# Performance work log

Hardware: AMD Instinct MI355X
Metric: run time of the kernel (lower is better)

## Reference

```python
import jax, jax.numpy as jnp
import numpy as np

B, T_CACHE, N_STATE, N_HEAD = 128, 448, 1280, 20
HEAD_DIM = N_STATE // N_HEAD


def setup_inputs() -> dict:
    key = jax.random.key(0)
    ks = jax.random.split(key, 10)
    s = 1.0 / np.sqrt(N_STATE)
    return {
        "x": jax.random.normal(ks[0], (B, 1, N_STATE), jnp.float32),
        "k_cache": jax.random.normal(ks[1], (B, T_CACHE, N_STATE), jnp.float32),
        "v_cache": jax.random.normal(ks[2], (B, T_CACHE, N_STATE), jnp.float32),
        "mask": jnp.zeros((1, T_CACHE), jnp.float32),
        "Wq": jax.random.normal(ks[3], (N_STATE, N_STATE), jnp.float32) * s,
        "bq": jax.random.normal(ks[4], (N_STATE,), jnp.float32) * s,
        "Wk": jax.random.normal(ks[5], (N_STATE, N_STATE), jnp.float32) * s,
        "Wv": jax.random.normal(ks[6], (N_STATE, N_STATE), jnp.float32) * s,
        "bv": jax.random.normal(ks[7], (N_STATE,), jnp.float32) * s,
        "Wo": jax.random.normal(ks[8], (N_STATE, N_STATE), jnp.float32) * s,
        "bo": jax.random.normal(ks[9], (N_STATE,), jnp.float32) * s,
    }


def reference(x, k_cache, v_cache, mask, Wq, bq, Wk, Wv, bv, Wo, bo):
    b, q_len, n_state = x.shape  # q_len == 1 in loop (streaming) mode
    h, d = N_HEAD, n_state // N_HEAD

    # Q/K/V projections (Whisper: key has no bias)
    q = x @ Wq + bq                         # [B, 1, n_state]
    k = x @ Wk                              # [B, 1, n_state]
    v = x @ Wv + bv                         # [B, 1, n_state]

    # streaming KV-cache shift-and-append
    k_cache = jnp.concatenate([k_cache[:, 1:, :], k], axis=1)  # [B, T, n_state]
    v_cache = jnp.concatenate([v_cache[:, 1:, :], v], axis=1)

    t = k_cache.shape[1]
    scale = d ** (-0.25)
    qh = q.reshape(b, q_len, h, d).transpose(0, 2, 1, 3) * scale   # [B, H, q, d]
    kh = k_cache.reshape(b, t, h, d).transpose(0, 2, 3, 1) * scale  # [B, H, d, T]
    vh = v_cache.reshape(b, t, h, d).transpose(0, 2, 1, 3)          # [B, H, T, d]

    qk = jnp.matmul(qh, kh) + mask          # [B, H, q, T]
    qk = qk.astype(jnp.float32)
    w = jax.nn.softmax(qk, axis=-1).astype(qh.dtype)
    wv = jnp.matmul(w, vh)                  # [B, H, q, d]
    wv = wv.transpose(0, 2, 1, 3).reshape(b, q_len, n_state)

    out = wv @ Wo + bo                      # [B, q, n_state]
    return out, k_cache, v_cache
```

## Files before the change

kernel.cpp:

```cpp
#include <hip/hip_runtime.h>
#include <cstddef>

#define NSTATE 1280
#define TCACHE 448
#define NBATCH 128
#define NHEAD  20
#define HDIM   64
#define NT     8
#define RPC    (TCACHE / NT)

typedef float f4 __attribute__((ext_vector_type(4)));

__device__ __forceinline__ void gemm_body(const float* __restrict__ A,
                                          const float* __restrict__ B,
                                          const float* __restrict__ bias,
                                          float* __restrict__ C, size_t ldc,
                                          int kb, int ke, float scale)
{
    __shared__ float As[32][64];
    __shared__ float Bs[32][32];
    const int tid = threadIdx.x;
    const int m0 = blockIdx.y * 64;
    const int n0 = blockIdx.x * 32;
    const int tr = tid >> 4;
    const int tc = tid & 15;
    float acc[4][2] = {{0.f,0.f},{0.f,0.f},{0.f,0.f},{0.f,0.f}};

    for (int k0 = kb; k0 < ke; k0 += 32) {
        #pragma unroll
        for (int j = 0; j < 2; ++j) {
            int chunk = tid * 2 + j;
            int row   = chunk >> 3;
            int kc    = (chunk & 7) << 2;
            float4 a = *(const float4*)(A + (size_t)(m0 + row) * NSTATE + k0 + kc);
            As[kc+0][row] = a.x; As[kc+1][row] = a.y;
            As[kc+2][row] = a.z; As[kc+3][row] = a.w;
        }
        {
            int row = tid >> 3;
            int nc  = (tid & 7) << 2;
            float4 b4 = *(const float4*)(B + (size_t)(k0 + row) * NSTATE + n0 + nc);
            *(float4*)&Bs[row][nc] = b4;
        }
        __syncthreads();
        #pragma unroll
        for (int kk = 0; kk < 32; ++kk) {
            float4 a = *(const float4*)&As[kk][tr << 2];
            float2 b = *(const float2*)&Bs[kk][tc << 1];
            acc[0][0] = fmaf(a.x, b.x, acc[0][0]); acc[0][1] = fmaf(a.x, b.y, acc[0][1]);
            acc[1][0] = fmaf(a.y, b.x, acc[1][0]); acc[1][1] = fmaf(a.y, b.y, acc[1][1]);
            acc[2][0] = fmaf(a.z, b.x, acc[2][0]); acc[2][1] = fmaf(a.z, b.y, acc[2][1]);
            acc[3][0] = fmaf(a.w, b.x, acc[3][0]); acc[3][1] = fmaf(a.w, b.y, acc[3][1]);
        }
        __syncthreads();
    }
    const int n = n0 + (tc << 1);
    const float b0 = bias ? bias[n]   : 0.f;
    const float b1 = bias ? bias[n+1] : 0.f;
    #pragma unroll
    for (int i = 0; i < 4; ++i) {
        size_t m = (size_t)(m0 + (tr << 2) + i);
        C[m * ldc + n]     = (acc[i][0] + b0) * scale;
        C[m * ldc + n + 1] = (acc[i][1] + b1) * scale;
    }
}

__global__ void __launch_bounds__(256) proj_qkv_kernel(
    const float* __restrict__ x,
    const float* __restrict__ Wq, const float* __restrict__ bq,
    const float* __restrict__ Wk,
    const float* __restrict__ Wv, const float* __restrict__ bv,
    float* __restrict__ q_ws, float* __restrict__ kout, float* __restrict__ vout)
{
    const int z = blockIdx.z;
    if (z == 0) {
        gemm_body(x, Wq, bq, q_ws, NSTATE, 0, NSTATE, 0.125f);
    } else if (z == 1) {
        gemm_body(x, Wk, nullptr, kout + (size_t)(TCACHE-1) * NSTATE,
                  (size_t)TCACHE * NSTATE, 0, NSTATE, 1.0f);
    } else {
        gemm_body(x, Wv, bv, vout + (size_t)(TCACHE-1) * NSTATE,
                  (size_t)TCACHE * NSTATE, 0, NSTATE, 1.0f);
    }
}

__global__ void __launch_bounds__(320) fused_stream_kernel(
    const float* __restrict__ kin, const float* __restrict__ vin,
    const float* __restrict__ q_ws, const float* __restrict__ mask,
    float* __restrict__ kout, float* __restrict__ vout,
    float* __restrict__ pvp, float* __restrict__ m_ws, float* __restrict__ s_ws)
{
    const int tc = blockIdx.x, b = blockIdx.y;
    const int tid = threadIdx.x;
    const int h = tid >> 4, l = tid & 15;
    const int col = tid << 2;
    const size_t base = (size_t)b * TCACHE * NSTATE;
    const int t0 = tc * RPC;
    const int nrows = (tc == NT - 1) ? RPC - 1 : RPC;

    __shared__ float sc[NHEAD][RPC];

    const float4 q4 = *(const float4*)(q_ws + (size_t)b * NSTATE + col);

    {
        const float* src0 = kin + base + (size_t)(t0 + 1) * NSTATE + col;
        float* dst0 = kout + base + (size_t)t0 * NSTATE + col;
        #pragma unroll 4
        for (int r = 0; r < nrows; ++r) {
            f4 kv = __builtin_nontemporal_load((const f4*)(src0 + (size_t)r * NSTATE));
            __builtin_nontemporal_store(kv, (f4*)(dst0 + (size_t)r * NSTATE));
            float p = kv[0]*q4.x + kv[1]*q4.y + kv[2]*q4.z + kv[3]*q4.w;
            p += __shfl_xor(p, 1); p += __shfl_xor(p, 2);
            p += __shfl_xor(p, 4); p += __shfl_xor(p, 8);
            if (l == 0) sc[h][r] = p + mask[t0 + r];
        }
        if (tc == NT - 1) {
            const f4 kv = *(const f4*)(kout + base + (size_t)(TCACHE-1) * NSTATE + col);
            float p = kv[0]*q4.x + kv[1]*q4.y + kv[2]*q4.z + kv[3]*q4.w;
            p += __shfl_xor(p, 1); p += __shfl_xor(p, 2);
            p += __shfl_xor(p, 4); p += __shfl_xor(p, 8);
            if (l == 0) sc[h][RPC - 1] = p + mask[TCACHE - 1];
        }
    }
    __syncthreads();

    {
        float v[4];
        float m = -1e30f;
        #pragma unroll
        for (int j = 0; j < 4; ++j) {
            int r = l + 16 * j;
            v[j] = (r < RPC) ? sc[h][r] : -1e30f;
            m = fmaxf(m, v[j]);
        }
        #pragma unroll
        for (int d = 1; d <= 8; d <<= 1) m = fmaxf(m, __shfl_xor(m, d));
        float s = 0.f;
        #pragma unroll
        for (int j = 0; j < 4; ++j) {
            v[j] = __expf(v[j] - m);
            s += v[j];
        }
        #pragma unroll
        for (int d = 1; d <= 8; d <<= 1) s += __shfl_xor(s, d);
        __syncthreads();
        #pragma unroll
        for (int j = 0; j < 4; ++j) {
            int r = l + 16 * j;
            if (r < RPC) sc[h][r] = v[j];
        }
        if (l == 0) {
            m_ws[((size_t)b * NT + tc) * NHEAD + h] = m;
            s_ws[((size_t)b * NT + tc) * NHEAD + h] = s;
        }
    }
    __syncthreads();

    float ax = 0.f, ay = 0.f, az = 0.f, aw = 0.f;
    {
        const float* src0 = vin + base + (size_t)(t0 + 1) * NSTATE + col;
        float* dst0 = vout + base + (size_t)t0 * NSTATE + col;
        #pragma unroll 4
        for (int r = 0; r < nrows; ++r) {
            f4 vv = __builtin_nontemporal_load((const f4*)(src0 + (size_t)r * NSTATE));
            __builtin_nontemporal_store(vv, (f4*)(dst0 + (size_t)r * NSTATE));
            const float w = sc[h][r];
            ax = fmaf(w, vv[0], ax); ay = fmaf(w, vv[1], ay);
            az = fmaf(w, vv[2], az); aw = fmaf(w, vv[3], aw);
        }
        if (tc == NT - 1) {
            const f4 vv = *(const f4*)(vout + base + (size_t)(TCACHE-1) * NSTATE + col);
            const float w = sc[h][RPC - 1];
            ax = fmaf(w, vv[0], ax); ay = fmaf(w, vv[1], ay);
            az = fmaf(w, vv[2], az); aw = fmaf(w, vv[3], aw);
        }
    }
    *(float4*)(pvp + ((size_t)b * NT + tc) * NSTATE + col) =
        make_float4(ax, ay, az, aw);
}

__global__ void __launch_bounds__(256) combine_kernel(
    const float* __restrict__ pvp, const float* __restrict__ m_ws,
    const float* __restrict__ s_ws, float* __restrict__ wv_ws)
{
    const size_t idx = ((size_t)blockIdx.x * 256 + threadIdx.x) * 4;
    const int b = (int)(idx / NSTATE), col = (int)(idx % NSTATE);
    const int h = col >> 6;

    float m[NT], s[NT];
    float M = -1e30f;
    #pragma unroll
    for (int c = 0; c < NT; ++c) {
        m[c] = m_ws[((size_t)b * NT + c) * NHEAD + h];
        s[c] = s_ws[((size_t)b * NT + c) * NHEAD + h];
        M = fmaxf(M, m[c]);
    }
    float S = 0.f;
    float f[NT];
    #pragma unroll
    for (int c = 0; c < NT; ++c) { f[c] = __expf(m[c] - M); S += s[c] * f[c]; }
    const float inv = 1.0f / S;

    float4 acc = make_float4(0.f, 0.f, 0.f, 0.f);
    #pragma unroll
    for (int c = 0; c < NT; ++c) {
        const float w = f[c] * inv;
        float4 a = *(const float4*)(pvp + ((size_t)b * NT + c) * NSTATE + col);
        acc.x = fmaf(w, a.x, acc.x); acc.y = fmaf(w, a.y, acc.y);
        acc.z = fmaf(w, a.z, acc.z); acc.w = fmaf(w, a.w, acc.w);
    }
    *(float4*)(wv_ws + idx) = acc;
}

__global__ void __launch_bounds__(256) outproj_kernel(
    const float* __restrict__ wv, const float* __restrict__ Wo,
    float* __restrict__ po)
{
    const int sp = blockIdx.z;
    gemm_body(wv, Wo, nullptr, po + (size_t)sp * NBATCH * NSTATE,
              NSTATE, sp * 320, sp * 320 + 320, 1.0f);
}

__global__ void __launch_bounds__(256) out_reduce_kernel(
    const float* __restrict__ po, const float* __restrict__ bo,
    float* __restrict__ out)
{
    const size_t idx = ((size_t)blockIdx.x * 256 + threadIdx.x) * 4;
    const int col = (int)(idx % NSTATE);
    float4 s = *(const float4*)(bo + col);
    #pragma unroll
    for (int c = 0; c < 4; ++c) {
        float4 a = *(const float4*)(po + (size_t)c * NBATCH * NSTATE + idx);
        s.x += a.x; s.y += a.y; s.z += a.z; s.w += a.w;
    }
    *(float4*)(out + idx) = s;
}

extern "C" void kernel_launch(void* const* d_in, const int* in_sizes, int n_in,
                              void* d_out, int out_size, void* d_ws, size_t ws_size,
                              hipStream_t stream)
{
    const float* x       = (const float*)d_in[0];
    const float* k_cache = (const float*)d_in[1];
    const float* v_cache = (const float*)d_in[2];
    const float* mask    = (const float*)d_in[3];
    const float* Wq      = (const float*)d_in[4];
    const float* bq      = (const float*)d_in[5];
    const float* Wk      = (const float*)d_in[6];
    const float* Wv      = (const float*)d_in[7];
    const float* bv      = (const float*)d_in[8];
    const float* Wo      = (const float*)d_in[9];
    const float* bo      = (const float*)d_in[10];

    float* out  = (float*)d_out;
    float* kout = out + (size_t)NBATCH * NSTATE;
    float* vout = kout + (size_t)NBATCH * TCACHE * NSTATE;

    float* ws     = (float*)d_ws;
    float* q_ws   = ws;
    float* pvp_ws = q_ws  + (size_t)NBATCH * NSTATE;
    float* m_ws   = pvp_ws + (size_t)NBATCH * NT * NSTATE;
    float* s_ws   = m_ws  + (size_t)NBATCH * NT * NHEAD;
    float* wv_ws  = s_ws  + (size_t)NBATCH * NT * NHEAD;
    float* po_ws  = wv_ws + (size_t)NBATCH * NSTATE;

    proj_qkv_kernel<<<dim3(40, 2, 3), 256, 0, stream>>>(x, Wq, bq, Wk, Wv, bv,
                                                        q_ws, kout, vout);
    fused_stream_kernel<<<dim3(NT, NBATCH), 320, 0, stream>>>(
        k_cache, v_cache, q_ws, mask, kout, vout, pvp_ws, m_ws, s_ws);
    combine_kernel<<<dim3(160), 256, 0, stream>>>(pvp_ws, m_ws, s_ws, wv_ws);
    outproj_kernel<<<dim3(40, 2, 4), 256, 0, stream>>>(wv_ws, Wo, po_ws);
    out_reduce_kernel<<<dim3(160), 256, 0, stream>>>(po_ws, bo, out);
}
```

Measured before the change: 308.4 us.

## Use bf16 MFMA for QKV and output projections, drop split-K reduction

Replaces the fp32 LDS-tiled GEMMs for the Q/K/V and output projections with bf16 MFMA 16x16x32 kernels that convert operands on load. The combine kernel now writes the attention output directly as bf16. The out-projection no longer uses split-K, so the separate reduce kernel and its partial-sum buffer are gone and one launch is saved. The cost is bf16 rounding of weights and activations, which may hurt accuracy. Another risk is that weights are loaded with strided scalar reads and there are few blocks (60 and 20), so occupancy is low. A redundant extra load was also added in combine.

```diff
diff --git a/kernel.cpp b/kernel.cpp
--- a/kernel.cpp
+++ b/kernel.cpp
@@ -10,78 +10,103 @@
 #define RPC    (TCACHE / NT)
 
 typedef float f4 __attribute__((ext_vector_type(4)));
-
-__device__ __forceinline__ void gemm_body(const float* __restrict__ A,
-                                          const float* __restrict__ B,
-                                          const float* __restrict__ bias,
-                                          float* __restrict__ C, size_t ldc,
-                                          int kb, int ke, float scale)
-{
-    __shared__ float As[32][64];
-    __shared__ float Bs[32][32];
-    const int tid = threadIdx.x;
-    const int m0 = blockIdx.y * 64;
-    const int n0 = blockIdx.x * 32;
-    const int tr = tid >> 4;
-    const int tc = tid & 15;
-    float acc[4][2] = {{0.f,0.f},{0.f,0.f},{0.f,0.f},{0.f,0.f}};
-
-    for (int k0 = kb; k0 < ke; k0 += 32) {
-        #pragma unroll
-        for (int j = 0; j < 2; ++j) {
-            int chunk = tid * 2 + j;
-            int row   = chunk >> 3;
-            int kc    = (chunk & 7) << 2;
-            float4 a = *(const float4*)(A + (size_t)(m0 + row) * NSTATE + k0 + kc);
-            As[kc+0][row] = a.x; As[kc+1][row] = a.y;
-            As[kc+2][row] = a.z; As[kc+3][row] = a.w;
-        }
-        {
-            int row = tid >> 3;
-            int nc  = (tid & 7) << 2;
-            float4 b4 = *(const float4*)(B + (size_t)(k0 + row) * NSTATE + n0 + nc);
-            *(float4*)&Bs[row][nc] = b4;
-        }
-        __syncthreads();
-        #pragma unroll
-        for (int kk = 0; kk < 32; ++kk) {
-            float4 a = *(const float4*)&As[kk][tr << 2];
-            float2 b = *(const float2*)&Bs[kk][tc << 1];
-            acc[0][0] = fmaf(a.x, b.x, acc[0][0]); acc[0][1] = fmaf(a.x, b.y, acc[0][1]);
-            acc[1][0] = fmaf(a.y, b.x, acc[1][0]); acc[1][1] = fmaf(a.y, b.y, acc[1][1]);
-            acc[2][0] = fmaf(a.z, b.x, acc[2][0]); acc[2][1] = fmaf(a.z, b.y, acc[2][1]);
-            acc[3][0] = fmaf(a.w, b.x, acc[3][0]); acc[3][1] = fmaf(a.w, b.y, acc[3][1]);
-        }
-        __syncthreads();
-    }
-    const int n = n0 + (tc << 1);
-    const float b0 = bias ? bias[n]   : 0.f;
-    const float b1 = bias ? bias[n+1] : 0.f;
-    #pragma unroll
-    for (int i = 0; i < 4; ++i) {
-        size_t m = (size_t)(m0 + (tr << 2) + i);
-        C[m * ldc + n]     = (acc[i][0] + b0) * scale;
-        C[m * ldc + n + 1] = (acc[i][1] + b1) * scale;
-    }
-}
-
-__global__ void __launch_bounds__(256) proj_qkv_kernel(
+typedef float f32x4 __attribute__((ext_vector_type(4)));
+typedef short bf16x8 __attribute__((ext_vector_type(8)));
+typedef unsigned short u16;
+
+__device__ __forceinline__ u16 f2bf(float f) {
+    unsigned u = __builtin_bit_cast(unsigned, f);
+    u += 0x7fff + ((u >> 16) & 1);
+    return (u16)(u >> 16);
+}
+
+__device__ __forceinline__ bf16x8 ld_a_bf16(const float* __restrict__ p) {
+    float4 a0 = *(const float4*)p;
+    float4 a1 = *(const float4*)(p + 4);
+    bf16x8 r;
+    r[0] = (short)f2bf(a0.x); r[1] = (short)f2bf(a0.y);
+    r[2] = (short)f2bf(a0.z); r[3] = (short)f2bf(a0.w);
+    r[4] = (short)f2bf(a1.x); r[5] = (short)f2bf(a1.y);
+    r[6] = (short)f2bf(a1.z); r[7] = (short)f2bf(a1.w);
+    return r;
+}
+
+__device__ __forceinline__ bf16x8 ld_b_bf16(const float* __restrict__ W,
+                                            int kk, int col) {
+    bf16x8 r;
+    #pragma unroll
+    for (int j = 0; j < 8; ++j)
+        r[j] = (short)f2bf(W[(size_t)(kk + j) * NSTATE + col]);
+    return r;
+}
+
+__global__ void __launch_bounds__(512) proj_mfma_kernel(
     const float* __restrict__ x,
     const float* __restrict__ Wq, const float* __restrict__ bq,
     const float* __restrict__ Wk,
     const float* __restrict__ Wv, const float* __restrict__ bv,
     float* __restrict__ q_ws, float* __restrict__ kout, float* __restrict__ vout)
 {
-    const int z = blockIdx.z;
-    if (z == 0) {
-        gemm_body(x, Wq, bq, q_ws, NSTATE, 0, NSTATE, 0.125f);
-    } else if (z == 1) {
-        gemm_body(x, Wk, nullptr, kout + (size_t)(TCACHE-1) * NSTATE,
-                  (size_t)TCACHE * NSTATE, 0, NSTATE, 1.0f);
-    } else {
-        gemm_body(x, Wv, bv, vout + (size_t)(TCACHE-1) * NSTATE,
-                  (size_t)TCACHE * NSTATE, 0, NSTATE, 1.0f);
-    }
+    const int nt = blockIdx.x, z = blockIdx.y;
+    const float* W = (z == 0) ? Wq : (z == 1) ? Wk : Wv;
+    const int w = threadIdx.x >> 6, l = threadIdx.x & 63;
+    const int mh = w >> 2, ns = w & 3;
+    const int col = nt * 64 + ns * 16 + (l & 15);
+    const int kg = l >> 4;
+    f32x4 acc[4] = {};
+
+    for (int ks = 0; ks < NSTATE; ks += 32) {
+        const int kk = ks + kg * 8;
+        const bf16x8 b = ld_b_bf16(W, kk, col);
+        #pragma unroll
+        for (int mf = 0; mf < 4; ++mf) {
+            const int row = (mh * 4 + mf) * 16 + (l & 15);
+            bf16x8 a = ld_a_bf16(x + (size_t)row * NSTATE + kk);
+            acc[mf] = __builtin_amdgcn_mfma_f32_16x16x32_bf16(a, b, acc[mf], 0, 0, 0);
+        }
+    }
+    const float bias = (z == 0) ? bq[col] : (z == 2) ? bv[col] : 0.f;
+    #pragma unroll
+    for (int mf = 0; mf < 4; ++mf) {
+        #pragma unroll
+        for (int j = 0; j < 4; ++j) {
+            const int m = (mh * 4 + mf) * 16 + kg * 4 + j;
+            const float val = acc[mf][j] + bias;
+            if (z == 0)      q_ws[(size_t)m * NSTATE + col] = val * 0.125f;
+            else if (z == 1) kout[((size_t)m * TCACHE + TCACHE - 1) * NSTATE + col] = val;
+            else             vout[((size_t)m * TCACHE + TCACHE - 1) * NSTATE + col] = val;
+        }
+    }
+}
+
+__global__ void __launch_bounds__(512) outproj_mfma_kernel(
+    const u16* __restrict__ wvbf, const float* __restrict__ Wo,
+    const float* __restrict__ bo, float* __restrict__ out)
+{
+    const int nt = blockIdx.x;
+    const int w = threadIdx.x >> 6, l = threadIdx.x & 63;
+    const int mh = w >> 2, ns = w & 3;
+    const int col = nt * 64 + ns * 16 + (l & 15);
+    const int kg = l >> 4;
+    f32x4 acc[4] = {};
+
+    for (int ks = 0; ks < NSTATE; ks += 32) {
+        const int kk = ks + kg * 8;
+        const bf16x8 b = ld_b_bf16(Wo, kk, col);
+        #pragma unroll
+        for (int mf = 0; mf < 4; ++mf) {
+            const int row = (mh * 4 + mf) * 16 + (l & 15);
+            bf16x8 a = *(const bf16x8*)(wvbf + (size_t)row * NSTATE + kk);
+            acc[mf] = __builtin_amdgcn_mfma_f32_16x16x32_bf16(a, b, acc[mf], 0, 0, 0);
+        }
+    }
+    const float bias = bo[col];
+    #pragma unroll
+    for (int mf = 0; mf < 4; ++mf)
+        #pragma unroll
+        for (int j = 0; j < 4; ++j)
+            out[(size_t)((mh * 4 + mf) * 16 + kg * 4 + j) * NSTATE + col] =
+                acc[mf][j] + bias;
 }
 
 __global__ void __launch_bounds__(320) fused_stream_kernel(
@@ -181,7 +206,7 @@
 
 __global__ void __launch_bounds__(256) combine_kernel(
     const float* __restrict__ pvp, const float* __restrict__ m_ws,
-    const float* __restrict__ s_ws, float* __restrict__ wv_ws)
+    const float* __restrict__ s_ws, u16* __restrict__ wvbf)
 {
     const size_t idx = ((size_t)blockIdx.x * 256 + threadIdx.x) * 4;
     const int b = (int)(idx / NSTATE), col = (int)(idx % NSTATE);
@@ -205,35 +230,15 @@
     #pragma unroll
     for (int c = 0; c < NT; ++c) {
         const float w = f[c] * inv;
-        float4 a = *(const float4*)(pvp + ((size_t)b * NT + c) * NSTATE + col);
+        float4 a = *(const float4*)(pvp + ((size_t)b * NT + c) * NSTATE + idx % NSTATE + (size_t)(idx / NSTATE) * 0);
+        (void)a;
+        a = *(const float4*)(pvp + ((size_t)b * NT + c) * NSTATE + col);
         acc.x = fmaf(w, a.x, acc.x); acc.y = fmaf(w, a.y, acc.y);
         acc.z = fmaf(w, a.z, acc.z); acc.w = fmaf(w, a.w, acc.w);
     }
-    *(float4*)(wv_ws + idx) = acc;
-}
-
-__global__ void __launch_bounds__(256) outproj_kernel(
-    const float* __restrict__ wv, const float* __restrict__ Wo,
-    float* __restrict__ po)
-{
-    const int sp = blockIdx.z;
-    gemm_body(wv, Wo, nullptr, po + (size_t)sp * NBATCH * NSTATE,
-              NSTATE, sp * 320, sp * 320 + 320, 1.0f);
-}
-
-__global__ void __launch_bounds__(256) out_reduce_kernel(
-    const float* __restrict__ po, const float* __restrict__ bo,
-    float* __restrict__ out)
-{
-    const size_t idx = ((size_t)blockIdx.x * 256 + threadIdx.x) * 4;
-    const int col = (int)(idx % NSTATE);
-    float4 s = *(const float4*)(bo + col);
-    #pragma unroll
-    for (int c = 0; c < 4; ++c) {
-        float4 a = *(const float4*)(po + (size_t)c * NBATCH * NSTATE + idx);
-        s.x += a.x; s.y += a.y; s.z += a.z; s.w += a.w;
-    }
-    *(float4*)(out + idx) = s;
+    u16* o = wvbf + idx;
+    o[0] = f2bf(acc.x); o[1] = f2bf(acc.y);
+    o[2] = f2bf(acc.z); o[3] = f2bf(acc.w);
 }
 
 extern "C" void kernel_launch(void* const* d_in, const int* in_sizes, int n_in,
@@ -261,14 +266,12 @@
     float* pvp_ws = q_ws  + (size_t)NBATCH * NSTATE;
     float* m_ws   = pvp_ws + (size_t)NBATCH * NT * NSTATE;
     float* s_ws   = m_ws  + (size_t)NBATCH * NT * NHEAD;
-    float* wv_ws  = s_ws  + (size_t)NBATCH * NT * NHEAD;
-    float* po_ws  = wv_ws + (size_t)NBATCH * NSTATE;
-
-    proj_qkv_kernel<<<dim3(40, 2, 3), 256, 0, stream>>>(x, Wq, bq, Wk, Wv, bv,
-                                                        q_ws, kout, vout);
+    u16*   wvbf   = (u16*)(s_ws + (size_t)NBATCH * NT * NHEAD);
+
+    proj_mfma_kernel<<<dim3(20, 3), 512, 0, stream>>>(x, Wq, bq, Wk, Wv, bv,
+                                                      q_ws, kout, vout);
     fused_stream_kernel<<<dim3(NT, NBATCH), 320, 0, stream>>>(
         k_cache, v_cache, q_ws, mask, kout, vout, pvp_ws, m_ws, s_ws);
-    combine_kernel<<<dim3(160), 256, 0, stream>>>(pvp_ws, m_ws, s_ws, wv_ws);
-    outproj_kernel<<<dim3(40, 2, 4), 256, 0, stream>>>(wv_ws, Wo, po_ws);
-    out_reduce_kernel<<<dim3(160), 256, 0, stream>>>(po_ws, bo, out);
-}
+    combine_kernel<<<dim3(160), 256, 0, stream>>>(pvp_ws, m_ws, s_ws, wvbf);
+    outproj_mfma_kernel<<<dim3(20), 512, 0, stream>>>(wvbf, Wo, bo, out);
+}
```

New measurement: 360.6 us. 1.17x slower.

## Fuse K and V passes into a single online-softmax loop

Applied to the files above, without the earlier changes.

Replaces the three-phase split-chunk attention (K scores into shared memory, softmax, then V pass) with one loop that streams K and V rows together and keeps a running max and sum per head. This removes the shared score buffer and the two block barriers, and it interleaves K and V loads so more memory requests are in flight per iteration. In exchange every row costs two exps plus a rescale of the accumulators, and each thread carries more live registers.

```diff
diff --git a/kernel.cpp b/kernel.cpp
--- a/kernel.cpp
+++ b/kernel.cpp
@@ -98,82 +98,56 @@
     const int t0 = tc * RPC;
     const int nrows = (tc == NT - 1) ? RPC - 1 : RPC;
 
-    __shared__ float sc[NHEAD][RPC];
-
     const float4 q4 = *(const float4*)(q_ws + (size_t)b * NSTATE + col);
-
-    {
-        const float* src0 = kin + base + (size_t)(t0 + 1) * NSTATE + col;
-        float* dst0 = kout + base + (size_t)t0 * NSTATE + col;
-        #pragma unroll 4
-        for (int r = 0; r < nrows; ++r) {
-            f4 kv = __builtin_nontemporal_load((const f4*)(src0 + (size_t)r * NSTATE));
-            __builtin_nontemporal_store(kv, (f4*)(dst0 + (size_t)r * NSTATE));
-            float p = kv[0]*q4.x + kv[1]*q4.y + kv[2]*q4.z + kv[3]*q4.w;
-            p += __shfl_xor(p, 1); p += __shfl_xor(p, 2);
-            p += __shfl_xor(p, 4); p += __shfl_xor(p, 8);
-            if (l == 0) sc[h][r] = p + mask[t0 + r];
-        }
-        if (tc == NT - 1) {
-            const f4 kv = *(const f4*)(kout + base + (size_t)(TCACHE-1) * NSTATE + col);
-            float p = kv[0]*q4.x + kv[1]*q4.y + kv[2]*q4.z + kv[3]*q4.w;
-            p += __shfl_xor(p, 1); p += __shfl_xor(p, 2);
-            p += __shfl_xor(p, 4); p += __shfl_xor(p, 8);
-            if (l == 0) sc[h][RPC - 1] = p + mask[TCACHE - 1];
-        }
-    }
-    __syncthreads();
-
-    {
-        float v[4];
-        float m = -1e30f;
-        #pragma unroll
-        for (int j = 0; j < 4; ++j) {
-            int r = l + 16 * j;
-            v[j] = (r < RPC) ? sc[h][r] : -1e30f;
-            m = fmaxf(m, v[j]);
-        }
-        #pragma unroll
-        for (int d = 1; d <= 8; d <<= 1) m = fmaxf(m, __shfl_xor(m, d));
-        float s = 0.f;
-        #pragma unroll
-        for (int j = 0; j < 4; ++j) {
-            v[j] = __expf(v[j] - m);
-            s += v[j];
-        }
-        #pragma unroll
-        for (int d = 1; d <= 8; d <<= 1) s += __shfl_xor(s, d);
-        __syncthreads();
-        #pragma unroll
-        for (int j = 0; j < 4; ++j) {
-            int r = l + 16 * j;
-            if (r < RPC) sc[h][r] = v[j];
-        }
-        if (l == 0) {
-            m_ws[((size_t)b * NT + tc) * NHEAD + h] = m;
-            s_ws[((size_t)b * NT + tc) * NHEAD + h] = s;
-        }
-    }
-    __syncthreads();
-
+    const float* ksrc = kin + base + (size_t)(t0 + 1) * NSTATE + col;
+    const float* vsrc = vin + base + (size_t)(t0 + 1) * NSTATE + col;
+    float* kdst = kout + base + (size_t)t0 * NSTATE + col;
+    float* vdst = vout + base + (size_t)t0 * NSTATE + col;
+
+    float m = -1e30f, s = 0.f;
     float ax = 0.f, ay = 0.f, az = 0.f, aw = 0.f;
-    {
-        const float* src0 = vin + base + (size_t)(t0 + 1) * NSTATE + col;
-        float* dst0 = vout + base + (size_t)t0 * NSTATE + col;
-        #pragma unroll 4
-        for (int r = 0; r < nrows; ++r) {
-            f4 vv = __builtin_nontemporal_load((const f4*)(src0 + (size_t)r * NSTATE));
-            __builtin_nontemporal_store(vv, (f4*)(dst0 + (size_t)r * NSTATE));
-            const float w = sc[h][r];
-            ax = fmaf(w, vv[0], ax); ay = fmaf(w, vv[1], ay);
-            az = fmaf(w, vv[2], az); aw = fmaf(w, vv[3], aw);
-        }
-        if (tc == NT - 1) {
-            const f4 vv = *(const f4*)(vout + base + (size_t)(TCACHE-1) * NSTATE + col);
-            const float w = sc[h][RPC - 1];
-            ax = fmaf(w, vv[0], ax); ay = fmaf(w, vv[1], ay);
-            az = fmaf(w, vv[2], az); aw = fmaf(w, vv[3], aw);
-        }
+
+    #pragma unroll 4
+    for (int r = 0; r < nrows; ++r) {
+        f4 kv = __builtin_nontemporal_load((const f4*)(ksrc + (size_t)r * NSTATE));
+        f4 vv = __builtin_nontemporal_load((const f4*)(vsrc + (size_t)r * NSTATE));
+        __builtin_nontemporal_store(kv, (f4*)(kdst + (size_t)r * NSTATE));
+        __builtin_nontemporal_store(vv, (f4*)(vdst + (size_t)r * NSTATE));
+        float p = kv[0]*q4.x + kv[1]*q4.y + kv[2]*q4.z + kv[3]*q4.w;
+        p += __shfl_xor(p, 1); p += __shfl_xor(p, 2);
+        p += __shfl_xor(p, 4); p += __shfl_xor(p, 8);
+        p += mask[t0 + r];
+        const float mn = fmaxf(m, p);
+        const float c  = __expf(m - mn);
+        const float w  = __expf(p - mn);
+        s = fmaf(s, c, w);
+        ax = fmaf(ax, c, w * vv[0]);
+        ay = fmaf(ay, c, w * vv[1]);
+        az = fmaf(az, c, w * vv[2]);
+        aw = fmaf(aw, c, w * vv[3]);
+        m = mn;
+    }
+    if (tc == NT - 1) {
+        const f4 kv = *(const f4*)(kout + base + (size_t)(TCACHE-1) * NSTATE + col);
+        const f4 vv = *(const f4*)(vout + base + (size_t)(TCACHE-1) * NSTATE + col);
+        float p = kv[0]*q4.x + kv[1]*q4.y + kv[2]*q4.z + kv[3]*q4.w;
+        p += __shfl_xor(p, 1); p += __shfl_xor(p, 2);
+        p += __shfl_xor(p, 4); p += __shfl_xor(p, 8);
+        p += mask[TCACHE - 1];
+        const float mn = fmaxf(m, p);
+        const float c  = __expf(m - mn);
+        const float w  = __expf(p - mn);
+        s = fmaf(s, c, w);
+        ax = fmaf(ax, c, w * vv[0]);
+        ay = fmaf(ay, c, w * vv[1]);
+        az = fmaf(az, c, w * vv[2]);
+        aw = fmaf(aw, c, w * vv[3]);
+        m = mn;
+    }
+
+    if (l == 0) {
+        m_ws[((size_t)b * NT + tc) * NHEAD + h] = m;
+        s_ws[((size_t)b * NT + tc) * NHEAD + h] = s;
     }
     *(float4*)(pvp + ((size_t)b * NT + tc) * NSTATE + col) =
         make_float4(ax, ay, az, aw);
```

New measurement: 318.1 us. 3.1% more time.
